# Optimization experiments

Measured on AMD Instinct MI355X. Metric: run time of the kernel, lower is better.

Reference implementation:

```python
import jax, jax.numpy as jnp
import numpy as np

B, D, T = 32, 256, 2048
L, K = 8, 1024


def setup_inputs() -> dict:
    key = jax.random.key(0)
    k1, k2 = jax.random.split(key)
    x = jax.random.normal(k1, (B, D, T), dtype=jnp.float32)
    codebooks = jax.random.normal(k2, (L, K, D), dtype=jnp.float32)
    return {"x": x, "codebooks": codebooks}


def reference(x, codebooks):
    """Residual VQ: per layer, cdist + argmin + gather, subtract, accumulate.

    x: (B, D, T) latents; codebooks: (L, K, D).
    Returns (output (B, D, T), indices (B, L, T)).
    """
    b, d, t = x.shape
    r0 = jnp.transpose(x, (0, 2, 1)).reshape(-1, d)  # (N, D), N = B*T

    def step(residual, W):
        # squared euclidean distance: |r|^2 - 2 r.W^T + |W|^2  -> (N, K)
        dist2 = (jnp.sum(residual * residual, axis=-1, keepdims=True)
                 - 2.0 * residual @ W.T
                 + jnp.sum(W * W, axis=-1))
        idx = jnp.argmin(dist2, axis=-1)          # (N,)
        q = W[idx]                                 # gather (N, D)
        return residual - q, (q, idx)

    _, (qs, idxs) = jax.lax.scan(step, r0, codebooks)
    out = jnp.sum(qs, axis=0).reshape(b, t, d)     # sum over layers
    out = jnp.transpose(out, (0, 2, 1))            # (B, D, T)
    indices = jnp.transpose(idxs.reshape(codebooks.shape[0], b, t), (1, 0, 2))  # (B, L, T)
    return out, indices
```

## Files before the change

### kernel.cpp

```cpp
#include <hip/hip_runtime.h>
#include <cmath>

constexpr int Bb = 32, Dd = 256, Tt = 2048, Ll = 8, Kk = 1024;
constexpr int VT = 64;
constexpr int KT = 64;
constexpr int ROWU = 264;
constexpr int HALF_USH = KT * ROWU;
constexpr int TILE_BYTES = 2 * HALF_USH * 2;
constexpr int CHUNKS = TILE_BYTES / 16 / 64;

typedef __attribute__((ext_vector_type(8))) short short8;
typedef __attribute__((ext_vector_type(4))) float f32x4;

__device__ __forceinline__ ushort f2bf(float x) {
    union { float f; uint32_t u; } v{x};
    uint32_t r = v.u + 0x7fffu + ((v.u >> 16) & 1u);
    return (ushort)(r >> 16);
}
__device__ __forceinline__ float bf2f(ushort h) {
    union { uint32_t u; float f; } v{((uint32_t)h) << 16};
    return v.f;
}
__device__ __forceinline__ void gl_lds16(const void* g, void* l) {
    __builtin_amdgcn_global_load_lds(
        (const __attribute__((address_space(1))) unsigned int*)g,
        (__attribute__((address_space(3))) unsigned int*)l, 16, 0, 0);
}

__global__ void prep_kernel(const float* __restrict__ cb, float* __restrict__ wn,
                            ushort* __restrict__ sp) {
    const int code = blockIdx.x;
    const int lane = threadIdx.x;
    const int l = code >> 10, kk = code & 1023, kt = kk >> 6, kr = kk & 63;
    const float4 v = ((const float4*)(cb + (size_t)code * Dd))[lane];
    float s = v.x * v.x + v.y * v.y + v.z * v.z + v.w * v.w;
#pragma unroll
    for (int off = 32; off > 0; off >>= 1) s += __shfl_down(s, off, 64);
    if (lane == 0) wn[code] = s;

    float f[4] = {v.x, v.y, v.z, v.w};
    ushort hs[4], ls[4];
#pragma unroll
    for (int i = 0; i < 4; ++i) {
        hs[i] = f2bf(f[i]);
        ls[i] = f2bf(f[i] - bf2f(hs[i]));
    }
    ushort* base = sp + (size_t)(l * 16 + kt) * (2 * HALF_USH) + kr * ROWU + lane * 4;
    *(ushort4*)base               = make_ushort4(hs[0], hs[1], hs[2], hs[3]);
    *(ushort4*)(base + HALF_USH)  = make_ushort4(ls[0], ls[1], ls[2], ls[3]);
}

__launch_bounds__(256, 2)
__global__ void rvq_kernel(const float* __restrict__ x, const float* __restrict__ cb,
                           const float* __restrict__ wn, const ushort* __restrict__ sp,
                           float* __restrict__ out, float* __restrict__ oidx) {
    __shared__ __align__(16) ushort Btile[2 * HALF_USH];
    __shared__ int   sidx[VT];
    __shared__ int   cnt[VT];
    __shared__ int   cand[VT * 32];

    const int tid = threadIdx.x;
    const int w = tid >> 6, lane = tid & 63;
    const int c = lane & 15;
    const int q = lane >> 4;
    const int b = blockIdx.x >> 5, t0 = (blockIdx.x & 31) * VT;
    const int myrow = 16 * w + c;
    const int t_a = t0 + myrow;

    float R_[8][8];
    {
        const float* xb = x + (size_t)b * Dd * Tt + t_a;
#pragma unroll
        for (int s = 0; s < 8; ++s)
#pragma unroll
            for (int j = 0; j < 8; ++j)
                R_[s][j] = xb[(size_t)(32 * s + 8 * q + j) * Tt];
    }

    for (int l = 0; l < Ll; ++l) {
        const float*  cbl = cb + (size_t)l * Kk * Dd;
        const float*  wnl = wn + l * Kk;
        const ushort* spl = sp + (size_t)l * 16 * (2 * HALF_USH);

        short8 ah[8], al[8];
#pragma unroll
        for (int s = 0; s < 8; ++s)
#pragma unroll
            for (int j = 0; j < 8; ++j) {
                float v = R_[s][j];
                ushort h = f2bf(v);
                ah[s][j] = (short)h;
                al[s][j] = (short)f2bf(v - bf2f(h));
            }

        float d1[4], d2[4]; int i1[4], i2[4];
#pragma unroll
        for (int i = 0; i < 4; ++i) { d1[i] = __builtin_inff(); d2[i] = __builtin_inff(); i1[i] = 0; i2[i] = 0; }

        for (int kt = 0; kt < 16; ++kt) {
            __syncthreads();
            {
                const char* gsrc = (const char*)spl + (size_t)kt * TILE_BYTES;
                char* ldst = (char*)Btile;
                for (int ch = w; ch < CHUNKS; ch += 4)
                    gl_lds16(gsrc + ch * 1024 + lane * 16, ldst + ch * 1024);
            }
            __syncthreads();

            float wnv[4];
#pragma unroll
            for (int sub = 0; sub < 4; ++sub) wnv[sub] = wnl[kt * 64 + sub * 16 + c];

            f32x4 hh[4], hl[4], lh[4];
#pragma unroll
            for (int sub = 0; sub < 4; ++sub) { hh[sub] = (f32x4)0.f; hl[sub] = (f32x4)0.f; lh[sub] = (f32x4)0.f; }

#pragma unroll
            for (int s = 0; s < 8; ++s) {
                const ushort* bp = Btile + s * 32 + q * 8;
                short8 bf[4];
#pragma unroll
                for (int sub = 0; sub < 4; ++sub)
                    bf[sub] = *(const short8*)(bp + (sub * 16 + c) * ROWU);
#pragma unroll
                for (int sub = 0; sub < 4; ++sub)
                    hh[sub] = __builtin_amdgcn_mfma_f32_16x16x32_bf16(ah[s], bf[sub], hh[sub], 0, 0, 0);
#pragma unroll
                for (int sub = 0; sub < 4; ++sub)
                    lh[sub] = __builtin_amdgcn_mfma_f32_16x16x32_bf16(al[s], bf[sub], lh[sub], 0, 0, 0);
#pragma unroll
                for (int sub = 0; sub < 4; ++sub)
                    bf[sub] = *(const short8*)(bp + HALF_USH + (sub * 16 + c) * ROWU);
#pragma unroll
                for (int sub = 0; sub < 4; ++sub)
                    hl[sub] = __builtin_amdgcn_mfma_f32_16x16x32_bf16(ah[s], bf[sub], hl[sub], 0, 0, 0);
            }
#pragma unroll
            for (int sub = 0; sub < 4; ++sub) {
                const int kbase = kt * 64 + sub * 16 + c;
#pragma unroll
                for (int i = 0; i < 4; ++i) {
                    float acc = hh[sub][i] + hl[sub][i] + lh[sub][i];
                    float d = fmaf(-2.f, acc, wnv[sub]);
                    bool lt1 = d < d1[i], lt2 = d < d2[i];
                    d2[i] = lt1 ? d1[i] : (lt2 ? d : d2[i]);
                    i2[i] = lt1 ? i1[i] : (lt2 ? kbase : i2[i]);
                    d1[i] = lt1 ? d : d1[i];
                    i1[i] = lt1 ? kbase : i1[i];
                }
            }
        }

        __syncthreads();
        float* Rcp = (float*)Btile;
        {
            float* dst = Rcp + myrow * ROWU + 8 * q;
#pragma unroll
            for (int s = 0; s < 8; ++s) {
                float4 lo4 = {R_[s][0], R_[s][1], R_[s][2], R_[s][3]};
                float4 hi4 = {R_[s][4], R_[s][5], R_[s][6], R_[s][7]};
                *(float4*)(dst + 32 * s)     = lo4;
                *(float4*)(dst + 32 * s + 4) = hi4;
            }
        }
        if (tid < VT) cnt[tid] = 0;

        float bmin[4];
#pragma unroll
        for (int i = 0; i < 4; ++i) {
            float md = d1[i];
#pragma unroll
            for (int off = 1; off < 16; off <<= 1) {
                float od = __shfl_xor(md, off, 64);
                md = od < md ? od : md;
            }
            bmin[i] = md;
        }
        __syncthreads();

#pragma unroll
        for (int i = 0; i < 4; ++i) {
            const int row = 16 * w + 4 * q + i;
            const float thr = bmin[i] + 0.20f;
            if (d1[i] <= thr) { int s_ = atomicAdd(&cnt[row], 1); cand[row * 32 + s_] = i1[i]; }
            if (d2[i] <= thr) { int s_ = atomicAdd(&cnt[row], 1); cand[row * 32 + s_] = i2[i]; }
        }
        __syncthreads();

        if (tid < VT) {
            const int row = tid;
            const int n = cnt[row];
            int bi = cand[row * 32];
            if (n > 1) {
                const float* rp = Rcp + row * ROWU;
                float rn = 0.f;
                for (int i = 0; i < Dd / 4; ++i) {
                    float4 r4 = *(const float4*)(rp + 4 * i);
                    rn += r4.x * r4.x + r4.y * r4.y + r4.z * r4.z + r4.w * r4.w;
                }
                float bd = __builtin_inff(); bi = 0x7fffffff;
                for (int j = 0; j < n; ++j) {
                    const int cc = cand[row * 32 + j];
                    const float* wp = cbl + (size_t)cc * Dd;
                    float dot = 0.f;
                    for (int d = 0; d < Dd; ++d)
                        dot = fmaf(rp[d], wp[d], dot);
                    const float dist = (rn - 2.0f * dot) + wnl[cc];
                    if (dist < bd || (dist == bd && cc < bi)) { bd = dist; bi = cc; }
                }
            }
            sidx[row] = bi;
            oidx[((size_t)b * Ll + l) * Tt + t0 + row] = (float)bi;
        }
        __syncthreads();

        {
            const int cc = sidx[myrow];
            const float* wp = cbl + (size_t)cc * Dd + 8 * q;
#pragma unroll
            for (int s = 0; s < 8; ++s) {
                float4 w0 = *(const float4*)(wp + 32 * s);
                float4 w1 = *(const float4*)(wp + 32 * s + 4);
                R_[s][0] -= w0.x; R_[s][1] -= w0.y; R_[s][2] -= w0.z; R_[s][3] -= w0.w;
                R_[s][4] -= w1.x; R_[s][5] -= w1.y; R_[s][6] -= w1.z; R_[s][7] -= w1.w;
            }
        }
    }

    {
        const float* xb = x + (size_t)b * Dd * Tt + t_a;
        float* ob = out + (size_t)b * Dd * Tt + t_a;
#pragma unroll
        for (int s = 0; s < 8; ++s)
#pragma unroll
            for (int j = 0; j < 8; ++j) {
                size_t off = (size_t)(32 * s + 8 * q + j) * Tt;
                ob[off] = xb[off] - R_[s][j];
            }
    }
}

extern "C" void kernel_launch(void* const* d_in, const int* in_sizes, int n_in,
                              void* d_out, int out_size, void* d_ws, size_t ws_size,
                              hipStream_t stream) {
    const float* x  = (const float*)d_in[0];
    const float* cb = (const float*)d_in[1];
    float* out  = (float*)d_out;
    float* oidx = out + (size_t)Bb * Dd * Tt;
    float*  wnbuf = (float*)d_ws;
    ushort* spbuf = (ushort*)((char*)d_ws + 32768);

    prep_kernel<<<Ll * Kk, 64, 0, stream>>>(cb, wnbuf, spbuf);
    rvq_kernel<<<(Bb * Tt) / VT, 256, 0, stream>>>(x, cb, wnbuf, spbuf, out, oidx);
}
```

Before: 1.147 ms.

## Drop codebook low-bf16 term, double-buffer codebook tiles, widen top-3 rescoring

The codebook is now stored as a single bf16 plane instead of a hi/lo split, which removes a third of the MFMAs and halves the tile bytes loaded per k-tile. Codebook tiles are double-buffered in LDS so the next tile's global-to-LDS load overlaps the current tile's compute, with one barrier per iteration instead of two. To make up for the lost precision, each lane keeps a top-3 list, the candidate threshold widens from 0.2 to 1.0, and the candidate buffer stride grows to 48. More rows will fall through to the scalar fp32 rescoring loop, and the 48-slot buffer could overflow if many candidates pass the threshold.

```diff
diff --git a/kernel.cpp b/kernel.cpp
--- a/kernel.cpp
+++ b/kernel.cpp
@@ -5,9 +5,10 @@
 constexpr int VT = 64;
 constexpr int KT = 64;
 constexpr int ROWU = 264;
-constexpr int HALF_USH = KT * ROWU;
-constexpr int TILE_BYTES = 2 * HALF_USH * 2;
-constexpr int CHUNKS = TILE_BYTES / 16 / 64;
+constexpr int TILE_USH = KT * ROWU;
+constexpr int TILE_BYTES = TILE_USH * 2;
+constexpr int CHUNKS = TILE_BYTES / 1024;
+constexpr int CSTR = 48;
 
 typedef __attribute__((ext_vector_type(8))) short short8;
 typedef __attribute__((ext_vector_type(4))) float f32x4;
@@ -39,25 +40,21 @@
     if (lane == 0) wn[code] = s;
 
     float f[4] = {v.x, v.y, v.z, v.w};
-    ushort hs[4], ls[4];
-#pragma unroll
-    for (int i = 0; i < 4; ++i) {
-        hs[i] = f2bf(f[i]);
-        ls[i] = f2bf(f[i] - bf2f(hs[i]));
-    }
-    ushort* base = sp + (size_t)(l * 16 + kt) * (2 * HALF_USH) + kr * ROWU + lane * 4;
-    *(ushort4*)base               = make_ushort4(hs[0], hs[1], hs[2], hs[3]);
-    *(ushort4*)(base + HALF_USH)  = make_ushort4(ls[0], ls[1], ls[2], ls[3]);
+    ushort hs[4];
+#pragma unroll
+    for (int i = 0; i < 4; ++i) hs[i] = f2bf(f[i]);
+    ushort* base = sp + (size_t)(l * 16 + kt) * TILE_USH + kr * ROWU + lane * 4;
+    *(ushort4*)base = make_ushort4(hs[0], hs[1], hs[2], hs[3]);
 }
 
 __launch_bounds__(256, 2)
 __global__ void rvq_kernel(const float* __restrict__ x, const float* __restrict__ cb,
                            const float* __restrict__ wn, const ushort* __restrict__ sp,
                            float* __restrict__ out, float* __restrict__ oidx) {
-    __shared__ __align__(16) ushort Btile[2 * HALF_USH];
+    __shared__ __align__(16) ushort Btile[2 * TILE_USH];
     __shared__ int   sidx[VT];
     __shared__ int   cnt[VT];
-    __shared__ int   cand[VT * 32];
+    __shared__ int   cand[VT * CSTR];
 
     const int tid = threadIdx.x;
     const int w = tid >> 6, lane = tid & 63;
@@ -80,7 +77,7 @@
     for (int l = 0; l < Ll; ++l) {
         const float*  cbl = cb + (size_t)l * Kk * Dd;
         const float*  wnl = wn + l * Kk;
-        const ushort* spl = sp + (size_t)l * 16 * (2 * HALF_USH);
+        const ushort* spl = sp + (size_t)l * 16 * TILE_USH;
 
         short8 ah[8], al[8];
 #pragma unroll
@@ -93,31 +90,38 @@
                 al[s][j] = (short)f2bf(v - bf2f(h));
             }
 
-        float d1[4], d2[4]; int i1[4], i2[4];
-#pragma unroll
-        for (int i = 0; i < 4; ++i) { d1[i] = __builtin_inff(); d2[i] = __builtin_inff(); i1[i] = 0; i2[i] = 0; }
-
+        float d1[4], d2[4], d3[4]; int i1[4], i2[4], i3[4];
+#pragma unroll
+        for (int i = 0; i < 4; ++i) {
+            d1[i] = __builtin_inff(); d2[i] = __builtin_inff(); d3[i] = __builtin_inff();
+            i1[i] = 0; i2[i] = 0; i3[i] = 0;
+        }
+
+        auto STAGE = [&](int kt, int buf) {
+            const char* gsrc = (const char*)spl + (size_t)kt * TILE_BYTES;
+            char* ldst = (char*)(Btile + buf * TILE_USH);
+            for (int ch = w; ch < CHUNKS; ch += 4)
+                gl_lds16(gsrc + ch * 1024 + lane * 16, ldst + ch * 1024);
+        };
+
+        STAGE(0, 0);
         for (int kt = 0; kt < 16; ++kt) {
             __syncthreads();
-            {
-                const char* gsrc = (const char*)spl + (size_t)kt * TILE_BYTES;
-                char* ldst = (char*)Btile;
-                for (int ch = w; ch < CHUNKS; ch += 4)
-                    gl_lds16(gsrc + ch * 1024 + lane * 16, ldst + ch * 1024);
-            }
-            __syncthreads();
+            if (kt < 15) STAGE(kt + 1, (kt + 1) & 1);
+
+            const ushort* bt = Btile + (kt & 1) * TILE_USH;
 
             float wnv[4];
 #pragma unroll
             for (int sub = 0; sub < 4; ++sub) wnv[sub] = wnl[kt * 64 + sub * 16 + c];
 
-            f32x4 hh[4], hl[4], lh[4];
-#pragma unroll
-            for (int sub = 0; sub < 4; ++sub) { hh[sub] = (f32x4)0.f; hl[sub] = (f32x4)0.f; lh[sub] = (f32x4)0.f; }
+            f32x4 hh[4], lh[4];
+#pragma unroll
+            for (int sub = 0; sub < 4; ++sub) { hh[sub] = (f32x4)0.f; lh[sub] = (f32x4)0.f; }
 
 #pragma unroll
             for (int s = 0; s < 8; ++s) {
-                const ushort* bp = Btile + s * 32 + q * 8;
+                const ushort* bp = bt + s * 32 + q * 8;
                 short8 bf[4];
 #pragma unroll
                 for (int sub = 0; sub < 4; ++sub)
@@ -128,21 +132,17 @@
 #pragma unroll
                 for (int sub = 0; sub < 4; ++sub)
                     lh[sub] = __builtin_amdgcn_mfma_f32_16x16x32_bf16(al[s], bf[sub], lh[sub], 0, 0, 0);
-#pragma unroll
-                for (int sub = 0; sub < 4; ++sub)
-                    bf[sub] = *(const short8*)(bp + HALF_USH + (sub * 16 + c) * ROWU);
-#pragma unroll
-                for (int sub = 0; sub < 4; ++sub)
-                    hl[sub] = __builtin_amdgcn_mfma_f32_16x16x32_bf16(ah[s], bf[sub], hl[sub], 0, 0, 0);
             }
 #pragma unroll
             for (int sub = 0; sub < 4; ++sub) {
                 const int kbase = kt * 64 + sub * 16 + c;
 #pragma unroll
                 for (int i = 0; i < 4; ++i) {
-                    float acc = hh[sub][i] + hl[sub][i] + lh[sub][i];
+                    float acc = hh[sub][i] + lh[sub][i];
                     float d = fmaf(-2.f, acc, wnv[sub]);
-                    bool lt1 = d < d1[i], lt2 = d < d2[i];
+                    bool lt1 = d < d1[i], lt2 = d < d2[i], lt3 = d < d3[i];
+                    d3[i] = lt2 ? d2[i] : (lt3 ? d : d3[i]);
+                    i3[i] = lt2 ? i2[i] : (lt3 ? kbase : i3[i]);
                     d2[i] = lt1 ? d1[i] : (lt2 ? d : d2[i]);
                     i2[i] = lt1 ? i1[i] : (lt2 ? kbase : i2[i]);
                     d1[i] = lt1 ? d : d1[i];
@@ -181,16 +181,17 @@
 #pragma unroll
         for (int i = 0; i < 4; ++i) {
             const int row = 16 * w + 4 * q + i;
-            const float thr = bmin[i] + 0.20f;
-            if (d1[i] <= thr) { int s_ = atomicAdd(&cnt[row], 1); cand[row * 32 + s_] = i1[i]; }
-            if (d2[i] <= thr) { int s_ = atomicAdd(&cnt[row], 1); cand[row * 32 + s_] = i2[i]; }
+            const float thr = bmin[i] + 1.0f;
+            if (d1[i] <= thr) { int s_ = atomicAdd(&cnt[row], 1); cand[row * CSTR + s_] = i1[i]; }
+            if (d2[i] <= thr) { int s_ = atomicAdd(&cnt[row], 1); cand[row * CSTR + s_] = i2[i]; }
+            if (d3[i] <= thr) { int s_ = atomicAdd(&cnt[row], 1); cand[row * CSTR + s_] = i3[i]; }
         }
         __syncthreads();
 
         if (tid < VT) {
             const int row = tid;
             const int n = cnt[row];
-            int bi = cand[row * 32];
+            int bi = cand[row * CSTR];
             if (n > 1) {
                 const float* rp = Rcp + row * ROWU;
                 float rn = 0.f;
@@ -200,7 +201,7 @@
                 }
                 float bd = __builtin_inff(); bi = 0x7fffffff;
                 for (int j = 0; j < n; ++j) {
-                    const int cc = cand[row * 32 + j];
+                    const int cc = cand[row * CSTR + j];
                     const float* wp = cbl + (size_t)cc * Dd;
                     float dot = 0.f;
                     for (int d = 0; d < Dd; ++d)
```

Result: faster. 976.7 us (-14.8%).
